# Optimization experiments

Hardware: AMD Instinct MI355X
Metric: run time of the kernel (lower is better)

## Reference

```python
import jax, jax.numpy as jnp
import numpy as np
from jax import lax

FEAT_STRIDE = 16
RATIOS = np.array([0.5, 1.0, 2.0], np.float32)
SCALES = np.array([8.0, 16.0, 32.0], np.float32)
PRE_NMS, POST_NMS = 6000, 300
NMS_THRESH, MIN_SIZE, SCALE = 0.7, 16.0, 1.0


def anchor_base():
    py = px = FEAT_STRIDE / 2.0
    base = np.zeros((9, 4), np.float32)
    for i, r in enumerate(RATIOS):
        for j, s in enumerate(SCALES):
            h = FEAT_STRIDE * s * np.sqrt(r)
            w = FEAT_STRIDE * s * np.sqrt(1.0 / r)
            base[i * 3 + j] = [px - w / 2.0, py - h / 2.0, px + w / 2.0, py + h / 2.0]
    return jnp.asarray(base)


def all_anchors(h, w):
    base = anchor_base()  # (9,4)
    sy = jnp.arange(h, dtype=jnp.float32) * FEAT_STRIDE
    sx = jnp.arange(w, dtype=jnp.float32) * FEAT_STRIDE
    yy, xx = jnp.meshgrid(sy, sx, indexing='ij')
    shift = jnp.stack([xx.ravel(), yy.ravel(), xx.ravel(), yy.ravel()], axis=1)  # (hw,4)
    return (shift[:, None, :] + base[None, :, :]).reshape(-1, 4)  # (hw*9,4)


def conv2d(x, w, b):
    y = lax.conv_general_dilated(x, w, (1, 1), 'SAME',
                                 dimension_numbers=('NCHW', 'OIHW', 'NCHW'))
    return y + b[None, :, None, None]


def loc2bbox(anchor, loc):
    aw = anchor[:, 2] - anchor[:, 0]
    ah = anchor[:, 3] - anchor[:, 1]
    ax = anchor[:, 0] + 0.5 * aw
    ay = anchor[:, 1] + 0.5 * ah
    cx = loc[:, 0] * aw + ax
    cy = loc[:, 1] * ah + ay
    w = jnp.exp(loc[:, 2]) * aw
    h = jnp.exp(loc[:, 3]) * ah
    return jnp.stack([cx - 0.5 * w, cy - 0.5 * h, cx + 0.5 * w, cy + 0.5 * h], axis=1)


def nms_fixed(boxes, scores):
    # top pre_nms by score, then greedy sequential NMS with fixed shapes
    s, order = lax.top_k(scores, PRE_NMS)
    b = boxes[order]
    areas = (b[:, 2] - b[:, 0]) * (b[:, 3] - b[:, 1])
    idx = jnp.arange(PRE_NMS)

    def body(i, keep):
        xx1 = jnp.maximum(b[i, 0], b[:, 0])
        yy1 = jnp.maximum(b[i, 1], b[:, 1])
        xx2 = jnp.minimum(b[i, 2], b[:, 2])
        yy2 = jnp.minimum(b[i, 3], b[:, 3])
        inter = jnp.clip(xx2 - xx1, 0.0) * jnp.clip(yy2 - yy1, 0.0)
        iou = inter / (areas[i] + areas - inter + 1e-9)
        suppress = (iou > NMS_THRESH) & (idx > i) & keep[i]
        return keep & ~suppress

    keep = lax.fori_loop(0, PRE_NMS, body, jnp.isfinite(s))
    vals, sel = lax.top_k(jnp.where(keep, s, -jnp.inf), POST_NMS)
    roi = b[sel]
    return jnp.where(jnp.isfinite(vals)[:, None], roi, 0.0)  # (POST_NMS,4)


def proposal(loc, fg, anchor, img_h, img_w):
    roi = loc2bbox(anchor, loc)
    roi = jnp.stack([jnp.clip(roi[:, 0], 0.0, img_w), jnp.clip(roi[:, 1], 0.0, img_h),
                     jnp.clip(roi[:, 2], 0.0, img_w), jnp.clip(roi[:, 3], 0.0, img_h)], axis=1)
    ms = MIN_SIZE * SCALE
    valid = ((roi[:, 2] - roi[:, 0]) >= ms) & ((roi[:, 3] - roi[:, 1]) >= ms)
    return nms_fixed(roi, jnp.where(valid, fg, -jnp.inf))


def setup_inputs() -> dict:
    key = jax.random.key(0)
    ks = jax.random.split(key, 4)
    return {
        'x': jax.random.normal(ks[0], (8, 512, 50, 76), jnp.float32),
        'conv1_w': jax.random.normal(ks[1], (512, 512, 3, 3), jnp.float32) * 0.01,
        'conv1_b': jnp.zeros((512,), jnp.float32),
        'score_w': jax.random.normal(ks[2], (18, 512, 1, 1), jnp.float32) * 0.01,
        'score_b': jnp.zeros((18,), jnp.float32),
        'loc_w': jax.random.normal(ks[3], (36, 512, 1, 1), jnp.float32) * 0.01,
        'loc_b': jnp.zeros((36,), jnp.float32),
        'img_h': 800,
        'img_w': 1216,
    }


def reference(x, conv1_w, conv1_b, score_w, score_b, loc_w, loc_b, img_h, img_w):
    b, c, h, w = x.shape
    anchor = all_anchors(h, w)  # (h*w*9,4)
    feat = jax.nn.relu(conv2d(x, conv1_w, conv1_b))
    rpn_locs = conv2d(feat, loc_w, loc_b).transpose(0, 2, 3, 1).reshape(b, -1, 4)
    rpn_scores = conv2d(feat, score_w, score_b).transpose(0, 2, 3, 1)
    sm = jax.nn.softmax(rpn_scores.reshape(b, h, w, 9, 2), axis=4)
    fg = sm[..., 1].reshape(b, -1)
    rpn_scores = rpn_scores.reshape(b, -1, 2)
    rois = jax.vmap(lambda l, f: proposal(l, f, anchor, float(img_h), float(img_w)))(rpn_locs, fg)
    rois = rois.reshape(-1, 4)  # (b*POST_NMS,4)
    return rpn_locs, rpn_scores, rois, anchor
```

## Files before the change

kernel.cpp:

```cpp
#include <hip/hip_runtime.h>
#include <stdint.h>
#include <math.h>

typedef unsigned long long u64;
typedef unsigned int u32;
typedef _Float16 half8 __attribute__((ext_vector_type(8)));
typedef float f32x4 __attribute__((ext_vector_type(4)));

#define CC   512
#define HH   50
#define WW2  76
#define PP   3800
#define NB   8
#define NA   34200
#define PRE  6000
#define POST 300
#define NPAD 8192
#define SHALF 4096
#define SCHUNK 1069


__device__ __forceinline__ u32 skey(float f) {
    u32 u = __float_as_uint(f);
    return (u & 0x80000000u) ? ~u : (u | 0x80000000u);
}

__device__ __forceinline__ float4 anchor_at(int p, int a) {
    const float rv[3] = {0.5f, 1.0f, 2.0f};
    const float sv[3] = {8.0f, 16.0f, 32.0f};
    int ri = a / 3, si = a % 3;
    float s16 = 16.0f * sv[si];
    float hh = s16 * sqrtf(rv[ri]);
    float ww = s16 * sqrtf(1.0f / rv[ri]);
    float bx1 = 8.0f - 0.5f * ww, by1 = 8.0f - 0.5f * hh;
    float bx2 = 8.0f + 0.5f * ww, by2 = 8.0f + 0.5f * hh;
    float sx = (float)((p % WW2) * 16);
    float sy = (float)((p / WW2) * 16);
    return make_float4(sx + bx1, sy + by1, sx + bx2, sy + by2);
}

__device__ __forceinline__ int lds_slot(int m, int j) {
    return (((m >> 4) * 64) + ((m & 15) ^ ((4 * (j & 1)) | (8 * (j >> 1)))) + (j << 4)) << 3;
}

__global__ void k_split_x(const float* __restrict__ x, _Float16* __restrict__ xh,
                          _Float16* __restrict__ xl) {
    __shared__ float S[32][33];
    int zim = blockIdx.z;
    int p0 = blockIdx.x * 32, c0 = blockIdx.y * 32;
    int tx = threadIdx.x, ty0 = threadIdx.y;
    const float* xi = x + (size_t)zim * CC * PP;
#pragma unroll
    for (int yy = 0; yy < 32; yy += 8) {
        int cty = c0 + ty0 + yy, ptx = p0 + tx;
        S[ty0 + yy][tx] = (ptx < PP) ? xi[(size_t)cty * PP + ptx] : 0.f;
    }
    __syncthreads();
#pragma unroll
    for (int yy = 0; yy < 32; yy += 8) {
        int p = p0 + ty0 + yy;
        if (p < PP) {
            float v = S[tx][ty0 + yy];
            _Float16 h = (_Float16)v;
            float r = v - (float)h;
            size_t o = (size_t)(zim * PP + p) * 512 + c0 + tx;
            xh[o] = h;
            xl[o] = (_Float16)(r * 2048.0f);
        }
    }
}

__global__ void k_split_wall(const float* __restrict__ w, _Float16* __restrict__ wh,
                             _Float16* __restrict__ wl,
                             const float* __restrict__ lw, const float* __restrict__ sw,
                             _Float16* __restrict__ wh2, _Float16* __restrict__ wl2) {
    if (blockIdx.x >= 512) {
        int row = blockIdx.x - 512;
        for (int k = threadIdx.x; k < 512; k += 256) {
            float v = (row < 36) ? lw[row * 512 + k]
                                 : (row < 54 ? sw[(row - 36) * 512 + k] : 0.f);
            _Float16 h = (_Float16)v;
            float r = v - (float)h;
            wh2[row * 512 + k] = h;
            wl2[row * 512 + k] = (_Float16)(r * 2048.0f);
        }
        return;
    }
    __shared__ float S[4608];
    int co = blockIdx.x;
    for (int t = threadIdx.x; t < 4608; t += 256) S[t] = w[(size_t)co * 4608 + t];
    __syncthreads();
    int g = co >> 4, nlo = co & 15;
    for (int e = threadIdx.x; e < 4608; e += 256) {
        int cc = e / 9, idx = e - cc * 9;
        float v = S[cc * 9 + idx];
        _Float16 h = (_Float16)v;
        float r = v - (float)h;
        int kk = (cc >> 5) * 9 + idx;
        int lane = ((cc >> 3) & 3) * 16 + nlo;
        int j = cc & 7;
        size_t d = (((size_t)g * 144 + kk) * 64 + lane) * 8 + j;
        wh[d] = h;
        wl[d] = (_Float16)(r * 2048.0f);
    }
}

__global__ __launch_bounds__(256, 2) void k_conv(
    const _Float16* __restrict__ xh, const _Float16* __restrict__ xl,
    const _Float16* __restrict__ whF, const _Float16* __restrict__ wlF,
    const float* __restrict__ bias, _Float16* __restrict__ fh,
    _Float16* __restrict__ fl, int imgbase)
{
    __shared__ _Float16 lds[2 * 8192];
    const int tid = threadIdx.x;
    const int L = blockIdx.x;
    const int X = L & 7, q = L >> 3;
    const int nt = X & 3;
    const int zim = (X >> 2) * 2 + (q >= 30 ? 1 : 0);
    const int mt = q - (q >= 30 ? 30 : 0);
    const int m0 = mt * 128, n0 = nt * 128;
    const _Float16* xhi = xh + (size_t)zim * CC * PP;
    const _Float16* xlo = xl + (size_t)zim * CC * PP;

    const int mA0 = tid >> 2, jA0 = tid & 3;
    const int mA1 = 64 + (tid >> 2);

    f32x4 acc[4][4], acc2[4][4];
#pragma unroll
    for (int i = 0; i < 4; ++i)
#pragma unroll
        for (int j = 0; j < 4; ++j) {
            acc[i][j] = f32x4{0.f, 0.f, 0.f, 0.f};
            acc2[i][j] = f32x4{0.f, 0.f, 0.f, 0.f};
        }

    uint4 pa0h, pa0l, pa1h, pa1l;

    auto ld_a = [&](int m, int idx, int c0, uint4& vh, uint4& vl) {
        int dy = idx / 3 - 1, dx = idx % 3 - 1;
        int p = m0 + m;
        int px = p % 76, py = p / 76;
        bool av = (p < PP) && ((unsigned)(py + dy) < 50u) && ((unsigned)(px + dx) < 76u);
        if (av) {
            size_t off = (size_t)(p + dy * 76 + dx) * 512 + c0 + jA0 * 8;
            vh = *(const uint4*)(xhi + off);
            vl = *(const uint4*)(xlo + off);
        } else {
            vh = make_uint4(0, 0, 0, 0);
            vl = make_uint4(0, 0, 0, 0);
        }
    };
    auto stage_load = [&](int kk) {
        int c9 = kk / 9;
        int idx = kk - c9 * 9;
        int c0 = c9 << 5;
        ld_a(mA0, idx, c0, pa0h, pa0l);
        ld_a(mA1, idx, c0, pa1h, pa1l);
    };
    const int sl0 = lds_slot(mA0, jA0);
    const int sl1 = lds_slot(mA1, jA0);
    auto stage_write = [&](int buf) {
        _Float16* Lp = lds + buf * 8192;
        *(uint4*)(Lp + sl0)        = pa0h;
        *(uint4*)(Lp + 4096 + sl0) = pa0l;
        *(uint4*)(Lp + sl1)        = pa1h;
        *(uint4*)(Lp + 4096 + sl1) = pa1l;
    };

    const int lane = tid & 63, wave = tid >> 6;
    const int wm = wave & 1, wn = wave >> 1;
    const int jr = lane >> 4;
    const int rd_off = (((lane & 15) ^ ((4 * (jr & 1)) | (8 * (jr >> 1)))) + (jr << 4)) << 3;
    const int g0 = nt * 8 + wn * 4;
    const size_t lane8 = (size_t)lane * 8;

    half8 b0h[4], b0l[4], b1h[4], b1l[4];
    auto load_b = [&](int kk, half8* bh_, half8* bl_) {
#pragma unroll
        for (int ni = 0; ni < 4; ++ni) {
            size_t off = (((size_t)(g0 + ni) * 144 + kk) * 64) * 8 + lane8;
            bh_[ni] = *(const half8*)(whF + off);
            bl_[ni] = *(const half8*)(wlF + off);
        }
    };

    auto compute = [&](int buf, const half8* bh, const half8* bl) {
        const _Float16* Lp = lds + buf * 8192;
        half8 ah[4], al[4];
#pragma unroll
        for (int mi = 0; mi < 4; ++mi) {
            int slot = (((wm * 4 + mi) * 64) << 3) + rd_off;
            ah[mi] = *(const half8*)(Lp + slot);
            al[mi] = *(const half8*)(Lp + 4096 + slot);
        }
#pragma unroll
        for (int ni = 0; ni < 4; ++ni) {
#pragma unroll
            for (int mi = 0; mi < 4; ++mi) {
                acc[mi][ni]  = __builtin_amdgcn_mfma_f32_16x16x32_f16(ah[mi], bh[ni], acc[mi][ni], 0, 0, 0);
                acc2[mi][ni] = __builtin_amdgcn_mfma_f32_16x16x32_f16(ah[mi], bl[ni], acc2[mi][ni], 0, 0, 0);
                acc2[mi][ni] = __builtin_amdgcn_mfma_f32_16x16x32_f16(al[mi], bh[ni], acc2[mi][ni], 0, 0, 0);
            }
        }
    };

    stage_load(0);
    stage_write(0);
    load_b(0, b0h, b0l);
    __syncthreads();
    for (int kk = 0; kk < 144; kk += 2) {
        stage_load(kk + 1);
        load_b(kk + 1, b1h, b1l);
        compute(0, b0h, b0l);
        stage_write(1);
        __syncthreads();
        if (kk + 2 < 144) {
            stage_load(kk + 2);
            load_b(kk + 2, b0h, b0l);
        }
        compute(1, b1h, b1l);
        if (kk + 2 < 144) stage_write(0);
        __syncthreads();
    }

    const int qq = lane >> 4, cl = lane & 15;
    const size_t rowbase = (size_t)(imgbase + zim) * PP;
#pragma unroll
    for (int ni = 0; ni < 4; ++ni) {
        int n = n0 + (wn * 4 + ni) * 16 + cl;
        float bs = bias[n];
#pragma unroll
        for (int mi = 0; mi < 4; ++mi) {
            int mb = m0 + (wm * 4 + mi) * 16 + qq * 4;
            if (mb < PP) {
#pragma unroll
                for (int r = 0; r < 4; ++r) {
                    float v = fmaxf(acc[mi][ni][r] + acc2[mi][ni][r] * (1.f / 2048.f) + bs, 0.f);
                    _Float16 h = (_Float16)v;
                    float rr = v - (float)h;
                    size_t o = (rowbase + mb + r) * 512 + n;
                    fh[o] = h;
                    fl[o] = (_Float16)(rr * 2048.0f);
                }
            }
        }
    }
}

__global__ __launch_bounds__(256) void k_hgemm_post(
    const _Float16* __restrict__ fh, const _Float16* __restrict__ fl,
    const _Float16* __restrict__ wh2, const _Float16* __restrict__ wl2,
    const float* __restrict__ lb, const float* __restrict__ sbias,
    const int* __restrict__ imh_p, const int* __restrict__ imw_p,
    float* __restrict__ out0, float* __restrict__ out1,
    float* __restrict__ boxes, float* __restrict__ scores,
    float* __restrict__ out3)
{
    const int img = blockIdx.y;
    const int p0 = blockIdx.x * 64;
    const int wave = threadIdx.x >> 6, lane = threadIdx.x & 63;
    const int q8 = (lane >> 4) * 8;
    int arow = img * PP + p0 + wave * 16 + (lane & 15);
    if (arow >= NB * PP) arow = NB * PP - 1;
    const _Float16* fhp = fh + (size_t)arow * 512 + q8;
    const _Float16* flp = fl + (size_t)arow * 512 + q8;
    const _Float16* bhp = wh2 + (size_t)(lane & 15) * 512 + q8;
    const _Float16* blp = wl2 + (size_t)(lane & 15) * 512 + q8;

    f32x4 acc[4], acc2[4];
#pragma unroll
    for (int j = 0; j < 4; ++j) {
        acc[j] = f32x4{0.f, 0.f, 0.f, 0.f};
        acc2[j] = f32x4{0.f, 0.f, 0.f, 0.f};
    }

#pragma unroll 4
    for (int k0 = 0; k0 < 512; k0 += 32) {
        half8 ah = *(const half8*)(fhp + k0);
        half8 al = *(const half8*)(flp + k0);
#pragma unroll
        for (int nf = 0; nf < 4; ++nf) {
            half8 bh = *(const half8*)(bhp + (size_t)nf * 16 * 512 + k0);
            half8 bl = *(const half8*)(blp + (size_t)nf * 16 * 512 + k0);
            acc[nf]  = __builtin_amdgcn_mfma_f32_16x16x32_f16(ah, bh, acc[nf], 0, 0, 0);
            acc2[nf] = __builtin_amdgcn_mfma_f32_16x16x32_f16(ah, bl, acc2[nf], 0, 0, 0);
            acc2[nf] = __builtin_amdgcn_mfma_f32_16x16x32_f16(al, bh, acc2[nf], 0, 0, 0);
        }
    }

    __shared__ float Ls[64][68];
    const int q = lane >> 4, cl = lane & 15;
#pragma unroll
    for (int nf = 0; nf < 4; ++nf) {
        int n = nf * 16 + cl;
        float bs = (n < 36) ? lb[n] : (n < 54 ? sbias[n - 36] : 0.f);
#pragma unroll
        for (int r = 0; r < 4; ++r) {
            int ml = wave * 16 + q * 4 + r;
            Ls[ml][n] = acc[nf][r] + acc2[nf][r] * (1.f / 2048.f) + bs;
        }
    }
    __syncthreads();

    const float fimh = (float)(*imh_p), fimw = (float)(*imw_p);
    for (int task = threadIdx.x; task < 576; task += 256) {
        int pl = task / 9, a = task - pl * 9;
        int p = p0 + pl;
        if (p >= PP) continue;
        float4 loc = *(const float4*)&Ls[pl][a * 4];
        float2 sc = make_float2(Ls[pl][36 + a * 2], Ls[pl][36 + a * 2 + 1]);
        size_t ai = (size_t)img * NA + (size_t)p * 9 + a;
        *(float4*)&out0[ai * 4] = loc;
        *(float2*)&out1[ai * 2] = sc;
        float mx = fmaxf(sc.x, sc.y);
        float e0 = expf(sc.x - mx), e1 = expf(sc.y - mx);
        float fg = e1 / (e0 + e1);
        float4 an = anchor_at(p, a);
        if (img == 0) ((float4*)out3)[p * 9 + a] = an;
        float aw = an.z - an.x, ah = an.w - an.y;
        float ax = an.x + 0.5f * aw, ay = an.y + 0.5f * ah;
        float cx = loc.x * aw + ax;
        float cy = loc.y * ah + ay;
        float wb = expf(loc.z) * aw, hb = expf(loc.w) * ah;
        float x1 = cx - 0.5f * wb, y1 = cy - 0.5f * hb;
        float x2 = cx + 0.5f * wb, y2 = cy + 0.5f * hb;
        x1 = fminf(fmaxf(x1, 0.f), fimw);
        x2 = fminf(fmaxf(x2, 0.f), fimw);
        y1 = fminf(fmaxf(y1, 0.f), fimh);
        y2 = fminf(fmaxf(y2, 0.f), fimh);
        bool valid = ((x2 - x1) >= 16.0f) && ((y2 - y1) >= 16.0f);
        ((float4*)boxes)[ai] = make_float4(x1, y1, x2, y2);
        scores[ai] = valid ? fg : -INFINITY;
    }
}


__global__ __launch_bounds__(256) void k_sel_histscan(
    const float* __restrict__ scores, u32* __restrict__ ghist,
    u32* __restrict__ gpref, u32* __restrict__ grem, u32* __restrict__ gdone,
    int sh, int pass)
{
    __shared__ u32 wh[4][256];
    __shared__ u32 A[256];
    __shared__ int s_last, s_d;
    const int img = blockIdx.y, blk = blockIdx.x;
    const int tid = threadIdx.x, wv = tid >> 6;
#pragma unroll
    for (int w = 0; w < 4; ++w) wh[w][tid] = 0;
    __syncthreads();
    const u32 pmask = (pass == 0) ? 0u : (0xFFFFFFFFu << (sh + 8));
    const u32 pref = (pass == 0) ? 0u : gpref[img];
    const float4* sc4 = (const float4*)(scores + (size_t)img * NA);
    const int e40 = blk * SCHUNK;
    const int e41 = min(e40 + SCHUNK, NA / 4);
    for (int e4 = e40 + tid; e4 < e41; e4 += 256) {
        float4 s4 = sc4[e4];
        u32 kv[4] = {skey(s4.x), skey(s4.y), skey(s4.z), skey(s4.w)};
#pragma unroll
        for (int v = 0; v < 4; ++v)
            if ((kv[v] & pmask) == pref) atomicAdd(&wh[wv][(kv[v] >> sh) & 255u], 1u);
    }
    __syncthreads();
    u32 s = wh[0][tid] + wh[1][tid] + wh[2][tid] + wh[3][tid];
    if (s) atomicAdd(&ghist[img * 256 + tid], s);
    __threadfence();
    __syncthreads();
    if (tid == 0) s_last = (atomicAdd(&gdone[pass * 8 + img], 1u) == 7u) ? 1 : 0;
    __syncthreads();
    if (!s_last) return;
    u32 h = atomicAdd(&ghist[img * 256 + tid], 0u);
    A[tid] = h;
    if (tid == 0) s_d = 0;
    __syncthreads();
    for (int off = 1; off < 256; off <<= 1) {
        u32 v = A[tid] + ((tid + off < 256) ? A[tid + off] : 0u);
        __syncthreads();
        A[tid] = v;
        __syncthreads();
    }
    const u32 rem = (pass == 0) ? (u32)PRE : grem[img];
    if (A[tid] >= rem) atomicMax(&s_d, tid);
    __syncthreads();
    if (tid == 0) {
        int d = s_d;
        u32 snext = (d < 255) ? A[d + 1] : 0u;
        u32 pv = (pass == 0) ? 0u : gpref[img];
        gpref[img] = pv | ((u32)d << sh);
        grem[img] = rem - snext;
    }
    ghist[img * 256 + tid] = 0;
}

__global__ __launch_bounds__(256) void k_sel_collect(
    const float* __restrict__ scores, const u32* __restrict__ gpref,
    u32* __restrict__ gccnt, u64* __restrict__ arr)
{
    __shared__ u64 lst[4288];
    __shared__ u32 s_c, s_base;
    const int img = blockIdx.y, blk = blockIdx.x;
    const int tid = threadIdx.x, lane = tid & 63;
    if (tid == 0) s_c = 0;
    __syncthreads();
    const u32 T = gpref[img];
    const float4* sc4 = (const float4*)(scores + (size_t)img * NA);
    const int e40 = blk * SCHUNK;
    const int e41 = min(e40 + SCHUNK, NA / 4);
    for (int e4 = e40 + tid; e4 < e41; e4 += 256) {
        float4 s4 = sc4[e4];
        u32 ks[4] = {skey(s4.x), skey(s4.y), skey(s4.z), skey(s4.w)};
#pragma unroll
        for (int v = 0; v < 4; ++v) {
            bool take = ks[v] >= T;
            u64 bal = __ballot(take);
            if (bal) {
                int leader = __builtin_ctzll(bal);
                u32 base = 0;
                if (lane == leader) base = atomicAdd(&s_c, (u32)__popcll(bal));
                base = (u32)__shfl((int)base, leader);
                if (take)
                    lst[base + (u32)__popcll(bal & ((1ull << lane) - 1ull))] =
                        ((u64)ks[v] << 32) | (u64)(~(u32)(e4 * 4 + v));
            }
        }
    }
    __syncthreads();
    if (tid == 0) s_base = atomicAdd(&gccnt[img], s_c);
    __syncthreads();
    const u32 base = s_base, c = s_c;
    u64* ar = arr + (size_t)img * NPAD;
    for (u32 t = tid; t < c; t += 256) {
        u32 pos = base + t;
        if (pos < NPAD) ar[pos] = lst[t];
    }
}

__global__ __launch_bounds__(1024) void k_sel_sort2(
    u64* __restrict__ arr, const u32* __restrict__ gccnt)
{
    __shared__ u64 a[SHALF];
    const int img = blockIdx.y, half = blockIdx.x;
    const int tid = threadIdx.x;
    u32 n = gccnt[img]; if (n > NPAD) n = NPAD;
    u64* ar = arr + (size_t)img * NPAD + (size_t)half * SHALF;
    const int base = half * SHALF;
    for (int t = tid; t < SHALF; t += 1024)
        a[t] = ((u32)(base + t) < n) ? ar[t] : 0ull;
    for (u32 size = 2; size <= SHALF; size <<= 1) {
        for (u32 stride = size >> 1; stride > 0; stride >>= 1) {
            __syncthreads();
            for (u32 t2 = tid; t2 < SHALF / 2; t2 += 1024) {
                u32 i = 2 * t2 - (t2 & (stride - 1));
                u32 j = i + stride;
                u64 x = a[i], y = a[j];
                bool desc = ((i & size) == 0);
                if (desc ? (x < y) : (x > y)) { a[i] = y; a[j] = x; }
            }
        }
    }
    __syncthreads();
    for (int t = tid; t < SHALF; t += 1024) ar[t] = a[t];
}

__global__ __launch_bounds__(1024) void k_sel_merge(
    const float* __restrict__ scores, const float4* __restrict__ boxes,
    const u64* __restrict__ arr,
    float* __restrict__ sb, float4* __restrict__ bbs, float* __restrict__ areas)
{
    const int img = blockIdx.y;
    const int t = blockIdx.x * 1024 + threadIdx.x;
    if (t >= PRE) return;
    const u64* A = arr + (size_t)img * NPAD;
    const u64* B = A + SHALF;
    int lo = (t > SHALF) ? (t - SHALF) : 0;
    int hi = (t < SHALF) ? t : SHALF;
    while (lo < hi) {
        int mid = (lo + hi) >> 1;
        if (A[mid] > B[t - 1 - mid]) lo = mid + 1; else hi = mid;
    }
    const int i = lo, j = t - lo;
    u64 va = (i < SHALF) ? A[i] : 0ull;
    u64 vb = (j < SHALF) ? B[j] : 0ull;
    u64 v = (va > vb) ? va : vb;
    u32 e = ~(u32)v;
    const float* sc = scores + (size_t)img * NA;
    float s = sc[e];
    float4 bx = boxes[(size_t)img * NA + e];
    sb[img * PRE + t] = s;
    bbs[img * PRE + t] = bx;
    areas[img * PRE + t] = (bx.z - bx.x) * (bx.w - bx.y);
}

__global__ __launch_bounds__(256) void k_scan(
    const float* __restrict__ sb, const float4* __restrict__ bbs,
    float* __restrict__ out2)
{
    const int img = blockIdx.x;
    const int tid = threadIdx.x;
    const int lane = tid & 63, wv = tid >> 6;
    __shared__ u64 alive[94];
    __shared__ int list[POST];
    __shared__ float4 kb[POST];
    __shared__ float ka[POST];
    __shared__ float4 wb4[64];
    __shared__ float wa[64];
    __shared__ u64 rowp[4][64];
    __shared__ u64 wred[4];
    __shared__ int s_n;

    for (int j0 = 0; j0 < 94 * 64; j0 += 256) {
        int j = j0 + tid;
        bool al = (j < PRE) && isfinite(sb[(size_t)img * PRE + j]);
        u64 bal = __ballot(al);
        if (lane == 0) alive[(j0 >> 6) + wv] = bal;
    }
    if (tid == 0) s_n = 0;
    __syncthreads();

    for (int w = 0; w < 94; ++w) {
        int n = s_n;
        if (n >= POST) break;
        if (tid < 64) {
            int j = w * 64 + tid;
            float4 b = (j < PRE) ? bbs[(size_t)img * PRE + j] : make_float4(0, 0, 0, 0);
            wb4[tid] = b;
            wa[tid] = (b.z - b.x) * (b.w - b.y);
        }
        __syncthreads();
        {
            int l = tid & 63, part = tid >> 6;
            float4 bl = wb4[l];
            float al_ = wa[l];
            u64 m = 0;
            int b0 = part * 16;
#pragma unroll 4
            for (int b = b0; b < b0 + 16; ++b) {
                float4 bj = wb4[b];
                float xx1 = fmaxf(bl.x, bj.x), yy1 = fmaxf(bl.y, bj.y);
                float xx2 = fminf(bl.z, bj.z), yy2 = fminf(bl.w, bj.w);
                float iw = fmaxf(xx2 - xx1, 0.f), ih2 = fmaxf(yy2 - yy1, 0.f);
                float inter = iw * ih2;
                float iou = inter / (al_ + wa[b] - inter + 1e-9f);
                if (iou > 0.7f) m |= (1ull << b);
            }
            rowp[part][l] = m;
        }
        u64 loc = 0;
        for (int t = tid; t < n; t += 256) {
            float4 kbx = kb[t];
            float kar = ka[t];
            u64 m = 0;
#pragma unroll 4
            for (int b = 0; b < 64; ++b) {
                float4 bj = wb4[b];
                float xx1 = fmaxf(kbx.x, bj.x), yy1 = fmaxf(kbx.y, bj.y);
                float xx2 = fminf(kbx.z, bj.z), yy2 = fminf(kbx.w, bj.w);
                float iw = fmaxf(xx2 - xx1, 0.f), ih2 = fmaxf(yy2 - yy1, 0.f);
                float inter = iw * ih2;
                float iou = inter / (kar + wa[b] - inter + 1e-9f);
                if (iou > 0.7f) m |= (1ull << b);
            }
            loc |= m;
        }
#pragma unroll
        for (int off = 32; off > 0; off >>= 1)
            loc |= __shfl_down(loc, off);
        if (lane == 0) wred[wv] = loc;
        __syncthreads();
        if (wv == 0) {
            u64 supp = wred[0] | wred[1] | wred[2] | wred[3];
            u64 myrow = rowp[0][lane] | rowp[1][lane] | rowp[2][lane] | rowp[3][lane];
            u64 cur = alive[w] & ~supp;
            u64 keptw = 0;
            while (cur) {
                int b = __builtin_ctzll(cur);
                keptw |= 1ull << b;
                u64 row = __shfl(myrow, b);
                u64 hi = (b >= 63) ? 0ull : (~0ull << (b + 1));
                cur &= ~row & hi;
            }
            if (lane == 0) {
                int nn = n;
                u64 bits = keptw;
                while (bits && nn < POST) {
                    int bb = __builtin_ctzll(bits);
                    bits &= bits - 1;
                    list[nn] = w * 64 + bb;
                    kb[nn] = wb4[bb];
                    ka[nn] = wa[bb];
                    ++nn;
                }
                s_n = nn;
            }
        }
        __syncthreads();
    }
    __syncthreads();
    int n = s_n;
    for (int e = tid; e < POST; e += 256) {
        float4 bx = (e < n) ? bbs[(size_t)img * PRE + list[e]] : make_float4(0, 0, 0, 0);
        *(float4*)&out2[((size_t)img * POST + e) * 4] = bx;
    }
}

extern "C" void kernel_launch(void* const* d_in, const int* in_sizes, int n_in,
                              void* d_out, int out_size, void* d_ws, size_t ws_size,
                              hipStream_t stream)
{
    const float* x     = (const float*)d_in[0];
    const float* w1    = (const float*)d_in[1];
    const float* b1    = (const float*)d_in[2];
    const float* sw    = (const float*)d_in[3];
    const float* sbias = (const float*)d_in[4];
    const float* lw    = (const float*)d_in[5];
    const float* lb    = (const float*)d_in[6];
    const int*   imh   = (const int*)d_in[7];
    const int*   imw   = (const int*)d_in[8];
    float* out = (float*)d_out;
    char* ws = (char*)d_ws;

    _Float16* wh2W = (_Float16*)(ws + 0);
    _Float16* wl2W = (_Float16*)(ws + 65536);
    _Float16* whW  = (_Float16*)(ws + 131072);
    _Float16* wlW  = (_Float16*)(ws + 4849664);
    _Float16* xhW  = (_Float16*)(ws + 9568256);
    _Float16* xlW  = (_Float16*)(ws + 25133056);
    float*    boxesW  = (float*)(ws + 17350656);
    float*    scoresW = (float*)(ws + 21728256);
    float*    sbW     = (float*)(ws + 22822656);
    float*    bbsW    = (float*)(ws + 23014656);
    float*    areasW  = (float*)(ws + 23782656);
    _Float16* fhW  = (_Float16*)(ws + 40697856);
    _Float16* flW  = (_Float16*)(ws + 71827456);
    u32*      ghistW  = (u32*)(ws + 109581056);
    u32*      gccntW  = (u32*)(ws + 109589248);
    u32*      gprefW  = (u32*)(ws + 109589280);
    u32*      gremW   = (u32*)(ws + 109589312);
    u32*      gdoneW  = (u32*)(ws + 109589344);
    u64*      arrW    = (u64*)(ws + 109597440);

    float* out0 = out;
    float* out1 = out + 1094400;
    float* out2 = out + 1641600;
    float* out3 = out + 1651200;

    hipMemsetAsync(ws + 109581056, 0, 8416, stream);

    hipLaunchKernelGGL(k_split_wall, dim3(576), dim3(256), 0, stream,
                       w1, whW, wlW, lw, sw, wh2W, wl2W);
    for (int b = 0; b < 2; ++b) {
        hipLaunchKernelGGL(k_split_x, dim3(119, 16, 4), dim3(32, 8), 0, stream,
                           x + (size_t)b * 4 * CC * PP, xhW, xlW);
        hipLaunchKernelGGL(k_conv, dim3(480), dim3(256), 0, stream,
                           xhW, xlW, whW, wlW, b1, fhW, flW, b * 4);
    }
    hipLaunchKernelGGL(k_hgemm_post, dim3(60, NB), dim3(256), 0, stream,
                       fhW, flW, wh2W, wl2W, lb, sbias, imh, imw,
                       out0, out1, boxesW, scoresW, out3);
    for (int pass = 0; pass < 4; ++pass) {
        int sh = 24 - 8 * pass;
        hipLaunchKernelGGL(k_sel_histscan, dim3(8, NB), dim3(256), 0, stream,
                           scoresW, ghistW, gprefW, gremW, gdoneW, sh, pass);
    }
    hipLaunchKernelGGL(k_sel_collect, dim3(8, NB), dim3(256), 0, stream,
                       scoresW, gprefW, gccntW, arrW);
    hipLaunchKernelGGL(k_sel_sort2, dim3(2, NB), dim3(1024), 0, stream,
                       arrW, gccntW);
    hipLaunchKernelGGL(k_sel_merge, dim3((PRE + 1023) / 1024, NB), dim3(1024), 0, stream,
                       scoresW, (const float4*)boxesW, arrW,
                       sbW, (float4*)bbsW, areasW);
    hipLaunchKernelGGL(k_scan, dim3(NB), dim3(256), 0, stream,
                       sbW, (const float4*)bbsW, out2);
}
```

Measured before the change: 821.9 us.

## Fuse radix-select passes into one persistent kernel; widen x split transpose

Merges the four radix histogram passes and the collect step into a single kernel. Blocks of the same image synchronise through global flag spin-waits instead of separate kernel launches, which removes five launches and their gaps. The fp32-to-fp16 hi/lo split of x also moves to 64x64 tiles with paired half stores to cut block count and store instructions. The spin-wait relies on all 64 blocks being co-resident, which holds on this GPU but is not guaranteed in general.

```diff
diff --git a/kernel.cpp b/kernel.cpp
--- a/kernel.cpp
+++ b/kernel.cpp
@@ -43,29 +43,38 @@
     return (((m >> 4) * 64) + ((m & 15) ^ ((4 * (j & 1)) | (8 * (j >> 1)))) + (j << 4)) << 3;
 }
 
-__global__ void k_split_x(const float* __restrict__ x, _Float16* __restrict__ xh,
-                          _Float16* __restrict__ xl) {
-    __shared__ float S[32][33];
-    int zim = blockIdx.z;
-    int p0 = blockIdx.x * 32, c0 = blockIdx.y * 32;
-    int tx = threadIdx.x, ty0 = threadIdx.y;
+__global__ __launch_bounds__(256) void k_split_x2(
+    const float* __restrict__ x, _Float16* __restrict__ xh, _Float16* __restrict__ xl)
+{
+    __shared__ float S[64][65];
+    const int zim = blockIdx.z;
+    const int p0 = blockIdx.x * 64, c0 = blockIdx.y * 64;
+    const int t = threadIdx.x;
     const float* xi = x + (size_t)zim * CC * PP;
-#pragma unroll
-    for (int yy = 0; yy < 32; yy += 8) {
-        int cty = c0 + ty0 + yy, ptx = p0 + tx;
-        S[ty0 + yy][tx] = (ptx < PP) ? xi[(size_t)cty * PP + ptx] : 0.f;
-    }
-    __syncthreads();
-#pragma unroll
-    for (int yy = 0; yy < 32; yy += 8) {
-        int p = p0 + ty0 + yy;
+    const int p_l = t & 63, c_b = t >> 6;
+#pragma unroll
+    for (int i = 0; i < 16; ++i) {
+        int c_l = c_b * 16 + i;
+        int p = p0 + p_l;
+        S[c_l][p_l] = (p < PP) ? xi[(size_t)(c0 + c_l) * PP + p] : 0.f;
+    }
+    __syncthreads();
+    const int c2 = t & 31, pg = t >> 5;
+#pragma unroll
+    for (int i = 0; i < 8; ++i) {
+        int pl2 = pg * 8 + i;
+        int p = p0 + pl2;
         if (p < PP) {
-            float v = S[tx][ty0 + yy];
-            _Float16 h = (_Float16)v;
-            float r = v - (float)h;
-            size_t o = (size_t)(zim * PP + p) * 512 + c0 + tx;
-            xh[o] = h;
-            xl[o] = (_Float16)(r * 2048.0f);
+            float v0 = S[2 * c2][pl2];
+            float v1 = S[2 * c2 + 1][pl2];
+            _Float16 h0 = (_Float16)v0, h1 = (_Float16)v1;
+            float r0 = v0 - (float)h0, r1 = v1 - (float)h1;
+            union { _Float16 f[2]; u32 u; } uh, ul;
+            uh.f[0] = h0; uh.f[1] = h1;
+            ul.f[0] = (_Float16)(r0 * 2048.0f); ul.f[1] = (_Float16)(r1 * 2048.0f);
+            size_t o = (size_t)(zim * PP + p) * 512 + c0 + 2 * c2;
+            *(u32*)(xh + o) = uh.u;
+            *(u32*)(xl + o) = ul.u;
         }
     }
 }
@@ -334,77 +343,76 @@
     }
 }
 
-
-__global__ __launch_bounds__(256) void k_sel_histscan(
+__global__ __launch_bounds__(256) void k_select_all(
     const float* __restrict__ scores, u32* __restrict__ ghist,
     u32* __restrict__ gpref, u32* __restrict__ grem, u32* __restrict__ gdone,
-    int sh, int pass)
+    u32* __restrict__ gflag, u32* __restrict__ gccnt, u64* __restrict__ arr)
 {
     __shared__ u32 wh[4][256];
     __shared__ u32 A[256];
+    __shared__ u64 lst[4288];
+    __shared__ u32 s_c, s_base;
     __shared__ int s_last, s_d;
     const int img = blockIdx.y, blk = blockIdx.x;
-    const int tid = threadIdx.x, wv = tid >> 6;
-#pragma unroll
-    for (int w = 0; w < 4; ++w) wh[w][tid] = 0;
-    __syncthreads();
-    const u32 pmask = (pass == 0) ? 0u : (0xFFFFFFFFu << (sh + 8));
-    const u32 pref = (pass == 0) ? 0u : gpref[img];
+    const int tid = threadIdx.x, wv = tid >> 6, lane = tid & 63;
     const float4* sc4 = (const float4*)(scores + (size_t)img * NA);
     const int e40 = blk * SCHUNK;
     const int e41 = min(e40 + SCHUNK, NA / 4);
-    for (int e4 = e40 + tid; e4 < e41; e4 += 256) {
-        float4 s4 = sc4[e4];
-        u32 kv[4] = {skey(s4.x), skey(s4.y), skey(s4.z), skey(s4.w)};
-#pragma unroll
-        for (int v = 0; v < 4; ++v)
-            if ((kv[v] & pmask) == pref) atomicAdd(&wh[wv][(kv[v] >> sh) & 255u], 1u);
-    }
-    __syncthreads();
-    u32 s = wh[0][tid] + wh[1][tid] + wh[2][tid] + wh[3][tid];
-    if (s) atomicAdd(&ghist[img * 256 + tid], s);
-    __threadfence();
-    __syncthreads();
-    if (tid == 0) s_last = (atomicAdd(&gdone[pass * 8 + img], 1u) == 7u) ? 1 : 0;
-    __syncthreads();
-    if (!s_last) return;
-    u32 h = atomicAdd(&ghist[img * 256 + tid], 0u);
-    A[tid] = h;
-    if (tid == 0) s_d = 0;
-    __syncthreads();
-    for (int off = 1; off < 256; off <<= 1) {
-        u32 v = A[tid] + ((tid + off < 256) ? A[tid + off] : 0u);
-        __syncthreads();
-        A[tid] = v;
-        __syncthreads();
-    }
-    const u32 rem = (pass == 0) ? (u32)PRE : grem[img];
-    if (A[tid] >= rem) atomicMax(&s_d, tid);
-    __syncthreads();
-    if (tid == 0) {
-        int d = s_d;
-        u32 snext = (d < 255) ? A[d + 1] : 0u;
-        u32 pv = (pass == 0) ? 0u : gpref[img];
-        gpref[img] = pv | ((u32)d << sh);
-        grem[img] = rem - snext;
-    }
-    ghist[img * 256 + tid] = 0;
-}
-
-__global__ __launch_bounds__(256) void k_sel_collect(
-    const float* __restrict__ scores, const u32* __restrict__ gpref,
-    u32* __restrict__ gccnt, u64* __restrict__ arr)
-{
-    __shared__ u64 lst[4288];
-    __shared__ u32 s_c, s_base;
-    const int img = blockIdx.y, blk = blockIdx.x;
-    const int tid = threadIdx.x, lane = tid & 63;
+
+    for (int pass = 0; pass < 4; ++pass) {
+        const int sh = 24 - 8 * pass;
+#pragma unroll
+        for (int w = 0; w < 4; ++w) wh[w][tid] = 0;
+        __syncthreads();
+        const u32 pmask = (pass == 0) ? 0u : (0xFFFFFFFFu << (sh + 8));
+        const u32 pref = (pass == 0) ? 0u : atomicAdd(&gpref[img], 0u);
+        for (int e4 = e40 + tid; e4 < e41; e4 += 256) {
+            float4 s4 = sc4[e4];
+            u32 kv[4] = {skey(s4.x), skey(s4.y), skey(s4.z), skey(s4.w)};
+#pragma unroll
+            for (int v = 0; v < 4; ++v)
+                if ((kv[v] & pmask) == pref) atomicAdd(&wh[wv][(kv[v] >> sh) & 255u], 1u);
+        }
+        __syncthreads();
+        u32 s = wh[0][tid] + wh[1][tid] + wh[2][tid] + wh[3][tid];
+        if (s) atomicAdd(&ghist[img * 256 + tid], s);
+        __threadfence();
+        __syncthreads();
+        if (tid == 0) s_last = (atomicAdd(&gdone[pass * 8 + img], 1u) == 7u) ? 1 : 0;
+        __syncthreads();
+        if (s_last) {
+            u32 h = atomicAdd(&ghist[img * 256 + tid], 0u);
+            A[tid] = h;
+            if (tid == 0) s_d = 0;
+            __syncthreads();
+            for (int off = 1; off < 256; off <<= 1) {
+                u32 v = A[tid] + ((tid + off < 256) ? A[tid + off] : 0u);
+                __syncthreads();
+                A[tid] = v;
+                __syncthreads();
+            }
+            const u32 rem = (pass == 0) ? (u32)PRE : atomicAdd(&grem[img], 0u);
+            if (A[tid] >= rem) atomicMax(&s_d, tid);
+            __syncthreads();
+            if (tid == 0) {
+                int d = s_d;
+                u32 snext = (d < 255) ? A[d + 1] : 0u;
+                u32 pv = (pass == 0) ? 0u : atomicAdd(&gpref[img], 0u);
+                atomicExch(&gpref[img], pv | ((u32)d << sh));
+                atomicExch(&grem[img], rem - snext);
+            }
+            atomicExch(&ghist[img * 256 + tid], 0u);
+            __threadfence();
+            __syncthreads();
+            if (tid == 0) atomicExch(&gflag[pass * 8 + img], 1u);
+        }
+        if (tid == 0) { while (atomicAdd(&gflag[pass * 8 + img], 0u) == 0u) {} }
+        __syncthreads();
+    }
+
     if (tid == 0) s_c = 0;
     __syncthreads();
-    const u32 T = gpref[img];
-    const float4* sc4 = (const float4*)(scores + (size_t)img * NA);
-    const int e40 = blk * SCHUNK;
-    const int e41 = min(e40 + SCHUNK, NA / 4);
+    const u32 T = atomicAdd(&gpref[img], 0u);
     for (int e4 = e40 + tid; e4 < e41; e4 += 256) {
         float4 s4 = sc4[e4];
         u32 ks[4] = {skey(s4.x), skey(s4.y), skey(s4.z), skey(s4.w)};
@@ -636,6 +644,7 @@
     u32*      gprefW  = (u32*)(ws + 109589280);
     u32*      gremW   = (u32*)(ws + 109589312);
     u32*      gdoneW  = (u32*)(ws + 109589344);
+    u32*      gflagW  = (u32*)(ws + 109589472);
     u64*      arrW    = (u64*)(ws + 109597440);
 
     float* out0 = out;
@@ -643,12 +652,12 @@
     float* out2 = out + 1641600;
     float* out3 = out + 1651200;
 
-    hipMemsetAsync(ws + 109581056, 0, 8416, stream);
+    hipMemsetAsync(ws + 109581056, 0, 8544, stream);
 
     hipLaunchKernelGGL(k_split_wall, dim3(576), dim3(256), 0, stream,
                        w1, whW, wlW, lw, sw, wh2W, wl2W);
     for (int b = 0; b < 2; ++b) {
-        hipLaunchKernelGGL(k_split_x, dim3(119, 16, 4), dim3(32, 8), 0, stream,
+        hipLaunchKernelGGL(k_split_x2, dim3(60, 8, 4), dim3(256), 0, stream,
                            x + (size_t)b * 4 * CC * PP, xhW, xlW);
         hipLaunchKernelGGL(k_conv, dim3(480), dim3(256), 0, stream,
                            xhW, xlW, whW, wlW, b1, fhW, flW, b * 4);
@@ -656,13 +665,9 @@
     hipLaunchKernelGGL(k_hgemm_post, dim3(60, NB), dim3(256), 0, stream,
                        fhW, flW, wh2W, wl2W, lb, sbias, imh, imw,
                        out0, out1, boxesW, scoresW, out3);
-    for (int pass = 0; pass < 4; ++pass) {
-        int sh = 24 - 8 * pass;
-        hipLaunchKernelGGL(k_sel_histscan, dim3(8, NB), dim3(256), 0, stream,
-                           scoresW, ghistW, gprefW, gremW, gdoneW, sh, pass);
-    }
-    hipLaunchKernelGGL(k_sel_collect, dim3(8, NB), dim3(256), 0, stream,
-                       scoresW, gprefW, gccntW, arrW);
+    hipLaunchKernelGGL(k_select_all, dim3(8, NB), dim3(256), 0, stream,
+                       scoresW, ghistW, gprefW, gremW, gdoneW, gflagW,
+                       gccntW, arrW);
     hipLaunchKernelGGL(k_sel_sort2, dim3(2, NB), dim3(1024), 0, stream,
                        arrW, gccntW);
     hipLaunchKernelGGL(k_sel_merge, dim3((PRE + 1023) / 1024, NB), dim3(1024), 0, stream,
```

New measurement: 831.5 us. About the same (+1.2%).
